# Kernel tuning notes

Hardware: AMD Instinct MI355X
Metric: run time of the kernel (lower is better)

Reference implementation:

```python
import jax, jax.numpy as jnp
import numpy as np

MAX_REL_POS = 1024


def rel_to_abs(x):
    """Music Transformer skew: [b,h,l,l] rel logits -> abs-position logits."""
    b, h, l, _ = x.shape
    x = jnp.pad(x, ((0, 0), (0, 0), (0, 0), (1, 0)))  # pad left of last dim
    x = x.reshape(b, h, l + 1, l)
    return x[:, :, 1:l + 1, :l]


def get_rel_embeddings(embed, seq_len):
    m = embed.shape[0]
    pad_len = max(seq_len - m, 0)
    start = max(m - seq_len, 0)
    padded = jnp.pad(embed, ((pad_len, 0), (0, 0)))
    return padded[start:, :]  # [seq_len, d]


def setup_inputs() -> dict:
    key = jax.random.key(0)
    kq, kk, kv, kr = jax.random.split(key, 4)
    B, H, L, D = 2, 8, 2048, 64
    # scale q so logits are O(1) (realistic attention magnitudes)
    q = jax.random.normal(kq, (B, H, L, D), dtype=jnp.float32) * (1.0 / np.sqrt(D))
    k = jax.random.normal(kk, (B, H, L, D), dtype=jnp.float32)
    v = jax.random.normal(kv, (B, H, L, D), dtype=jnp.float32)
    rel_keys_weight = jax.random.normal(kr, (MAX_REL_POS, D), dtype=jnp.float32)
    # causal mask: True = masked (masked_fill semantics)
    mask = jnp.triu(jnp.ones((L, L), dtype=bool), k=1)[None, None]
    return {"q": q, "k": k, "v": v, "rel_keys_weight": rel_keys_weight, "mask": mask}


def reference(q, k, v, rel_keys_weight, mask):
    L = q.shape[2]
    logits = jnp.einsum('bhqd,bhkd->bhqk', q, k)
    rel_keys = get_rel_embeddings(rel_keys_weight, L)          # [L, D]
    rel_logits = jnp.einsum('bhqd,md->bhqm', q, rel_keys)      # [B,H,L,L]
    logits = logits + rel_to_abs(rel_logits)
    logits = jnp.where(mask, -jnp.inf, logits)
    weights = jax.nn.softmax(logits, axis=3)
    output = jnp.matmul(weights, v)
    return (output, weights)
```

## Files before the change

kernel.cpp:

```cpp
#include <hip/hip_runtime.h>
#include <hip/hip_bf16.h>

typedef short bf16x8 __attribute__((ext_vector_type(8)));
typedef float f32x4  __attribute__((ext_vector_type(4)));

#define SEQ   2048
#define HD    64
#define LDT   72
#define TSTR  84
#define GROWS 192
#define OUT0  (16 * SEQ * HD)

__device__ __forceinline__ short f2bf(float x) {
    unsigned u = __float_as_uint(x);
    unsigned r = u + 0x7fffu + ((u >> 16) & 1u);
    return (short)(r >> 16);
}

struct F16 { float4 a[4]; };

__device__ __forceinline__ void cvt8(const float4& x, const float4& y, bf16x8& p) {
    p[0] = f2bf(x.x); p[1] = f2bf(x.y); p[2] = f2bf(x.z); p[3] = f2bf(x.w);
    p[4] = f2bf(y.x); p[5] = f2bf(y.y); p[6] = f2bf(y.z); p[7] = f2bf(y.w);
}

__device__ __forceinline__ void issue64(const float* __restrict__ base, int tid, F16& f) {
    const int r = tid >> 2, cg = tid & 3;
    const float4* src = (const float4*)(base + (size_t)r * HD + cg * 16);
#pragma unroll
    for (int t = 0; t < 4; ++t) f.a[t] = src[t];
}
__device__ __forceinline__ void write64(short* __restrict__ dst, int tid, const F16& f) {
    const int r = tid >> 2, cg = tid & 3;
    bf16x8 p0, p1;
    cvt8(f.a[0], f.a[1], p0);
    cvt8(f.a[2], f.a[3], p1);
    *(bf16x8*)&dst[r * LDT + cg * 16]     = p0;
    *(bf16x8*)&dst[r * LDT + cg * 16 + 8] = p1;
}

__device__ __forceinline__ void issueG(const float* __restrict__ eg, int tid, int etop, F16& f) {
    const int r = tid >> 2, cg = tid & 3;
    const int e = etop - r;
    if (e >= 0 && e < 1024) {
        const float4* src = (const float4*)(eg + (size_t)e * HD + cg * 16);
#pragma unroll
        for (int t = 0; t < 4; ++t) f.a[t] = src[t];
    } else {
        const float4 z = make_float4(0.f, 0.f, 0.f, 0.f);
#pragma unroll
        for (int t = 0; t < 4; ++t) f.a[t] = z;
    }
}
__device__ __forceinline__ void writeG(short* __restrict__ Gr, int tid, int sbn, const F16& f) {
    const int r = tid >> 2, cg = tid & 3;
    int sl = r + sbn; if (sl >= GROWS) sl -= GROWS;
    bf16x8 p0, p1;
    cvt8(f.a[0], f.a[1], p0);
    cvt8(f.a[2], f.a[3], p1);
    *(bf16x8*)&Gr[sl * LDT + cg * 16]     = p0;
    *(bf16x8*)&Gr[sl * LDT + cg * 16 + 8] = p1;
}

__device__ __forceinline__ void stageG_full(const float* __restrict__ eg, short* __restrict__ Gr,
                                            int tid, int i0) {
    const int dd = tid >> 1, hf = tid & 1;
    const int e = 1086 - i0 - dd;
    int sl = dd + 128; if (sl >= GROWS) sl -= GROWS;
    short* dst = &Gr[sl * LDT + hf * 32];
    if (e >= 0 && e < 1024) {
        const float4* src = (const float4*)(eg + (size_t)e * HD + hf * 32);
#pragma unroll
        for (int u = 0; u < 4; ++u) {
            bf16x8 p; cvt8(src[2 * u], src[2 * u + 1], p);
            *(bf16x8*)&dst[u * 8] = p;
        }
    } else {
        bf16x8 z = {0, 0, 0, 0, 0, 0, 0, 0};
#pragma unroll
        for (int u = 0; u < 4; ++u) *(bf16x8*)&dst[u * 8] = z;
    }
}

__device__ __forceinline__ void issueV(const float* __restrict__ vbase, int tid, F16& f) {
    const int r = tid & 63, cg = tid >> 6;
    const float4* src = (const float4*)(vbase + (size_t)r * HD + cg * 16);
#pragma unroll
    for (int t = 0; t < 4; ++t) f.a[t] = src[t];
}
__device__ __forceinline__ void writeV(short* __restrict__ Vt, int tid, const F16& f) {
    const int r = tid & 63, cg = tid >> 6;
    const float* ff = (const float*)&f.a[0];
#pragma unroll
    for (int t = 0; t < 16; ++t)
        Vt[(cg * 16 + t) * LDT + r] = f2bf(ff[t]);
}

__device__ __forceinline__ void compute_sc(const bf16x8* aq, const short* __restrict__ Ks,
                                           const short* __restrict__ Gr, int sb,
                                           int wv, int qd, int c, int lane,
                                           f32x4* sc, bool diag) {
    f32x4 tc[5];
    const f32x4 zz = {0.f, 0.f, 0.f, 0.f};
#pragma unroll
    for (int ct = 0; ct < 4; ++ct) sc[ct] = zz;
#pragma unroll
    for (int dt = 0; dt < 5; ++dt) tc[dt] = zz;
    int sl[5];
#pragma unroll
    for (int dt = 0; dt < 5; ++dt) {
        int s0 = (wv + dt) * 16 + sb + c;
        if (s0 >= GROWS) s0 -= GROWS;
        sl[dt] = s0 * LDT;
    }
#pragma unroll
    for (int s = 0; s < 2; ++s) {
        bf16x8 a = aq[s];
#pragma unroll
        for (int ct = 0; ct < 4; ++ct) {
            bf16x8 b = *(const bf16x8*)&Ks[(ct * 16 + c) * LDT + s * 32 + qd * 8];
            sc[ct] = __builtin_amdgcn_mfma_f32_16x16x32_bf16(a, b, sc[ct], 0, 0, 0);
        }
#pragma unroll
        for (int dt = 0; dt < 5; ++dt) {
            bf16x8 g = *(const bf16x8*)&Gr[sl[dt] + s * 32 + qd * 8];
            tc[dt] = __builtin_amdgcn_mfma_f32_16x16x32_bf16(a, g, tc[dt], 0, 0, 0);
        }
    }
#pragma unroll
    for (int rg = 0; rg < 4; ++rg) {
        const int rl  = qd * 4 + rg;
        const int cp  = (rl + 63 - c) & 15;
        const int src = (lane & 48) | cp;
        const bool hi = (rl + 63 - cp) >= 64;
#pragma unroll
        for (int ct = 0; ct < 4; ++ct) {
            float vs = hi ? tc[4 - ct][rg] : tc[3 - ct][rg];
            float tr = __shfl(vs, src, 64);
            float sval = sc[ct][rg] + tr;
            if (diag && (ct * 16 + c > wv * 16 + rl)) sval = -3.0e38f;
            sc[ct][rg] = sval;
        }
    }
}

__global__ __launch_bounds__(256, 2)
void relattn(const float* __restrict__ qg, const float* __restrict__ kg,
             const float* __restrict__ vg, const float* __restrict__ eg,
             float* __restrict__ outp)
{
    __shared__ short Ks2[2][64 * LDT];
    __shared__ short Gr[GROWS * LDT];
    __shared__ short Vt2[2][64 * LDT];
    __shared__ short Ps[4 * 16 * TSTR];
    __shared__ float Ls[64];

    const int tid  = threadIdx.x;
    const int wv   = tid >> 6;
    const int lane = tid & 63;
    const int qd   = lane >> 4;
    const int c    = lane & 15;

    const int bh = blockIdx.x & 15;
    const int u  = blockIdx.x >> 4;
    const int qt = (u < 16) ? u : 47 - u;
    const int i0 = qt * 64;

    float* Wg = outp + OUT0;

    {
        const int z0v = (qt + 1) * 16;
        for (int r = 0; r < 64; ++r) {
            float4* dst = (float4*)(Wg + ((size_t)(bh * SEQ + i0 + r)) * SEQ);
            for (int jv = z0v + tid; jv < SEQ / 4; jv += 256)
                dst[jv] = make_float4(0.f, 0.f, 0.f, 0.f);
        }
    }

    {
        F16 fq; issue64(qg + ((size_t)(bh * SEQ + i0)) * HD, tid, fq);
        write64(Ks2[0], tid, fq);
    }
    __syncthreads();
    bf16x8 aq[2];
#pragma unroll
    for (int s = 0; s < 2; ++s)
        aq[s] = *(const bf16x8*)&Ks2[0][(wv * 16 + c) * LDT + s * 32 + qd * 8];
    __syncthreads();

    float lrun[4];
#pragma unroll
    for (int rg = 0; rg < 4; ++rg) lrun[rg] = 0.f;

    f32x4 ob[4];
    {
        const f32x4 zz = {0.f, 0.f, 0.f, 0.f};
#pragma unroll
        for (int dt = 0; dt < 4; ++dt) ob[dt] = zz;
    }

    {
        F16 fk; issue64(kg + ((size_t)(bh * SEQ)) * HD, tid, fk);
        write64(Ks2[0], tid, fk);
        stageG_full(eg, Gr, tid, i0);
        F16 fv; issueV(vg + ((size_t)(bh * SEQ)) * HD, tid, fv);
        writeV(Vt2[0], tid, fv);
    }
    __syncthreads();
    int sb = 128;
    short* Pw = &Ps[wv * 16 * TSTR];
    for (int kt = 0; kt <= qt; ++kt) {
        const int cur = kt & 1;
        const bool pf = kt < qt;
        const int sbn = (sb >= 64) ? sb - 64 : sb + 128;
        const int j0 = kt * 64;
        F16 fk, fg, fv;
        if (pf) {
            issue64(kg + ((size_t)(bh * SEQ + j0 + 64)) * HD, tid, fk);
            issueG(eg, tid, 1086 - i0 + j0 + 64, fg);
            issueV(vg + ((size_t)(bh * SEQ + j0 + 64)) * HD, tid, fv);
        }
        f32x4 sc[4];
        compute_sc(aq, Ks2[cur], Gr, sb, wv, qd, c, lane, sc, kt == qt);

#pragma unroll
        for (int rg = 0; rg < 4; ++rg) {
            const int rl = qd * 4 + rg;
            const int ig = i0 + wv * 16 + rl;
            float* wrow = Wg + ((size_t)(bh * SEQ + ig)) * SEQ + j0;
            float p[4];
#pragma unroll
            for (int ct = 0; ct < 4; ++ct) {
                p[ct] = __expf(sc[ct][rg]);
                wrow[ct * 16 + c] = p[ct];
                Pw[rl * TSTR + ct * 16 + c] = f2bf(p[ct]);
            }
            float ss = (p[0] + p[1]) + (p[2] + p[3]);
            ss += __shfl_xor(ss, 1);
            ss += __shfl_xor(ss, 2);
            ss += __shfl_xor(ss, 4);
            ss += __shfl_xor(ss, 8);
            lrun[rg] += ss;
        }

#pragma unroll
        for (int s = 0; s < 2; ++s) {
            bf16x8 ap = *(const bf16x8*)&Pw[c * TSTR + s * 32 + qd * 8];
#pragma unroll
            for (int dt = 0; dt < 4; ++dt) {
                bf16x8 bv = *(const bf16x8*)&Vt2[cur][(dt * 16 + c) * LDT + s * 32 + qd * 8];
                ob[dt] = __builtin_amdgcn_mfma_f32_16x16x32_bf16(ap, bv, ob[dt], 0, 0, 0);
            }
        }
        if (pf) {
            write64(Ks2[cur ^ 1], tid, fk);
            writeG(Gr, tid, sbn, fg);
            writeV(Vt2[cur ^ 1], tid, fv);
        }
        sb = sbn;
        __syncthreads();
    }

    float linv[4];
#pragma unroll
    for (int rg = 0; rg < 4; ++rg) linv[rg] = 1.0f / lrun[rg];

    if (c == 0) {
#pragma unroll
        for (int rg = 0; rg < 4; ++rg)
            Ls[wv * 16 + qd * 4 + rg] = linv[rg];
    }
    __syncthreads();

    {
        const int w16 = (qt + 1) * 16;
        for (int r = 0; r < 64; ++r) {
            const float s = Ls[r];
            float4* dst = (float4*)(Wg + ((size_t)(bh * SEQ + i0 + r)) * SEQ);
            for (int jv = tid; jv < w16; jv += 256) {
                float4 w = dst[jv];
                w.x *= s; w.y *= s; w.z *= s; w.w *= s;
                dst[jv] = w;
            }
        }
    }

#pragma unroll
    for (int dt = 0; dt < 4; ++dt)
#pragma unroll
        for (int rg = 0; rg < 4; ++rg) {
            const int ig = i0 + wv * 16 + qd * 4 + rg;
            outp[((size_t)(bh * SEQ + ig)) * HD + dt * 16 + c] = ob[dt][rg] * linv[rg];
        }
}

extern "C" void kernel_launch(void* const* d_in, const int* in_sizes, int n_in,
                              void* d_out, int out_size, void* d_ws, size_t ws_size,
                              hipStream_t stream) {
    const float* q = (const float*)d_in[0];
    const float* k = (const float*)d_in[1];
    const float* v = (const float*)d_in[2];
    const float* e = (const float*)d_in[3];
    float* out = (float*)d_out;
    hipLaunchKernelGGL(relattn, dim3(512), dim3(256), 0, stream, q, k, v, e, out);
}
```

Measured before the change: 448.5 us.

## Use two-pass softmax to write normalized weights directly, with key-split 512-thread blocks

The kernel now runs a first pass that only accumulates the exp row sums. A second pass recomputes the logits and writes already-normalized weights, which removes the read-modify-write rescale sweep over the large weights output. Each block now has 8 waves that split every 128-key block into two 64-key halves, and their partial sums and outputs are combined through LDS. Each block handles a complementary pair of query tiles to balance the causal workload. The cost is computing the QK and relative-logit MFMAs twice, plus one 512-thread block per CU with new LDS strides and setprio hints.

```diff
diff --git a/kernel.cpp b/kernel.cpp
--- a/kernel.cpp
+++ b/kernel.cpp
@@ -6,9 +6,10 @@
 
 #define SEQ   2048
 #define HD    64
-#define LDT   72
-#define TSTR  84
-#define GROWS 192
+#define LDT   66
+#define VSTR  130
+#define PSTR  66
+#define GROWS 320
 #define OUT0  (16 * SEQ * HD)
 
 __device__ __forceinline__ short f2bf(float x) {
@@ -17,20 +18,26 @@
     return (short)(r >> 16);
 }
 
-struct F16 { float4 a[4]; };
-
 __device__ __forceinline__ void cvt8(const float4& x, const float4& y, bf16x8& p) {
     p[0] = f2bf(x.x); p[1] = f2bf(x.y); p[2] = f2bf(x.z); p[3] = f2bf(x.w);
     p[4] = f2bf(y.x); p[5] = f2bf(y.y); p[6] = f2bf(y.z); p[7] = f2bf(y.w);
 }
 
-__device__ __forceinline__ void issue64(const float* __restrict__ base, int tid, F16& f) {
+__device__ __forceinline__ void barrier_lds() {
+    asm volatile("s_waitcnt lgkmcnt(0)" ::: "memory");
+    __builtin_amdgcn_s_barrier();
+    asm volatile("" ::: "memory");
+}
+
+struct F16 { float4 a[4]; };
+
+__device__ __forceinline__ void issueK(const float* __restrict__ base, int tid, F16& f) {
     const int r = tid >> 2, cg = tid & 3;
     const float4* src = (const float4*)(base + (size_t)r * HD + cg * 16);
 #pragma unroll
     for (int t = 0; t < 4; ++t) f.a[t] = src[t];
 }
-__device__ __forceinline__ void write64(short* __restrict__ dst, int tid, const F16& f) {
+__device__ __forceinline__ void writeK(short* __restrict__ dst, int tid, const F16& f) {
     const int r = tid >> 2, cg = tid & 3;
     bf16x8 p0, p1;
     cvt8(f.a[0], f.a[1], p0);
@@ -39,9 +46,9 @@
     *(bf16x8*)&dst[r * LDT + cg * 16 + 8] = p1;
 }
 
-__device__ __forceinline__ void issueG(const float* __restrict__ eg, int tid, int etop, F16& f) {
+__device__ __forceinline__ void issueG(const float* __restrict__ eg, int tid, int emax, F16& f) {
     const int r = tid >> 2, cg = tid & 3;
-    const int e = etop - r;
+    const int e = emax - r;
     if (e >= 0 && e < 1024) {
         const float4* src = (const float4*)(eg + (size_t)e * HD + cg * 16);
 #pragma unroll
@@ -63,62 +70,63 @@
 }
 
 __device__ __forceinline__ void stageG_full(const float* __restrict__ eg, short* __restrict__ Gr,
-                                            int tid, int i0) {
-    const int dd = tid >> 1, hf = tid & 1;
-    const int e = 1086 - i0 - dd;
-    int sl = dd + 128; if (sl >= GROWS) sl -= GROWS;
-    short* dst = &Gr[sl * LDT + hf * 32];
-    if (e >= 0 && e < 1024) {
-        const float4* src = (const float4*)(eg + (size_t)e * HD + hf * 32);
-#pragma unroll
-        for (int u = 0; u < 4; ++u) {
-            bf16x8 p; cvt8(src[2 * u], src[2 * u + 1], p);
-            *(bf16x8*)&dst[u * 8] = p;
-        }
-    } else {
-        bf16x8 z = {0, 0, 0, 0, 0, 0, 0, 0};
-#pragma unroll
-        for (int u = 0; u < 4; ++u) *(bf16x8*)&dst[u * 8] = z;
+                                            int tid, int emax0) {
+    const int r0 = tid >> 3, cg8 = tid & 7;
+#pragma unroll
+    for (int u = 0; u < 3; ++u) {
+        const int x = u * 64 + r0;
+        const int e = emax0 - x;
+        short* dst = &Gr[(x + 128) * LDT + cg8 * 8];
+        if (e >= 0 && e < 1024) {
+            const float4* src = (const float4*)(eg + (size_t)e * HD + cg8 * 8);
+            bf16x8 p; cvt8(src[0], src[1], p);
+            *(bf16x8*)dst = p;
+        } else {
+            bf16x8 z = {0, 0, 0, 0, 0, 0, 0, 0};
+            *(bf16x8*)dst = z;
+        }
     }
 }
 
 __device__ __forceinline__ void issueV(const float* __restrict__ vbase, int tid, F16& f) {
-    const int r = tid & 63, cg = tid >> 6;
-    const float4* src = (const float4*)(vbase + (size_t)r * HD + cg * 16);
+    const int r3 = tid & 127, dg = (tid >> 7) * 16;
+    const float4* src = (const float4*)(vbase + (size_t)r3 * HD + dg);
 #pragma unroll
     for (int t = 0; t < 4; ++t) f.a[t] = src[t];
 }
 __device__ __forceinline__ void writeV(short* __restrict__ Vt, int tid, const F16& f) {
-    const int r = tid & 63, cg = tid >> 6;
+    const int r3 = tid & 127, dg = (tid >> 7) * 16;
     const float* ff = (const float*)&f.a[0];
 #pragma unroll
     for (int t = 0; t < 16; ++t)
-        Vt[(cg * 16 + t) * LDT + r] = f2bf(ff[t]);
+        Vt[(dg + t) * VSTR + r3] = f2bf(ff[t]);
 }
 
 __device__ __forceinline__ void compute_sc(const bf16x8* aq, const short* __restrict__ Ks,
                                            const short* __restrict__ Gr, int sb,
-                                           int wv, int qd, int c, int lane,
-                                           f32x4* sc, bool diag) {
+                                           int w4, int jhh, int qd, int c, int lane,
+                                           f32x4* sc , bool diag, int igq, int jgq) {
     f32x4 tc[5];
     const f32x4 zz = {0.f, 0.f, 0.f, 0.f};
 #pragma unroll
     for (int ct = 0; ct < 4; ++ct) sc[ct] = zz;
 #pragma unroll
     for (int dt = 0; dt < 5; ++dt) tc[dt] = zz;
+    const int X0 = w4 * 16 - jhh + 64;
     int sl[5];
 #pragma unroll
     for (int dt = 0; dt < 5; ++dt) {
-        int s0 = (wv + dt) * 16 + sb + c;
+        int s0 = X0 + dt * 16 + c + sb;
         if (s0 >= GROWS) s0 -= GROWS;
         sl[dt] = s0 * LDT;
     }
+    __builtin_amdgcn_s_setprio(1);
 #pragma unroll
     for (int s = 0; s < 2; ++s) {
         bf16x8 a = aq[s];
 #pragma unroll
         for (int ct = 0; ct < 4; ++ct) {
-            bf16x8 b = *(const bf16x8*)&Ks[(ct * 16 + c) * LDT + s * 32 + qd * 8];
+            bf16x8 b = *(const bf16x8*)&Ks[(jhh + ct * 16 + c) * LDT + s * 32 + qd * 8];
             sc[ct] = __builtin_amdgcn_mfma_f32_16x16x32_bf16(a, b, sc[ct], 0, 0, 0);
         }
 #pragma unroll
@@ -127,171 +135,217 @@
             tc[dt] = __builtin_amdgcn_mfma_f32_16x16x32_bf16(a, g, tc[dt], 0, 0, 0);
         }
     }
+    __builtin_amdgcn_s_setprio(0);
 #pragma unroll
     for (int rg = 0; rg < 4; ++rg) {
         const int rl  = qd * 4 + rg;
-        const int cp  = (rl + 63 - c) & 15;
+        const int cp  = (rl + 15 - c) & 15;
         const int src = (lane & 48) | cp;
-        const bool hi = (rl + 63 - cp) >= 64;
+        const bool hi = rl > cp;
 #pragma unroll
         for (int ct = 0; ct < 4; ++ct) {
             float vs = hi ? tc[4 - ct][rg] : tc[3 - ct][rg];
             float tr = __shfl(vs, src, 64);
             float sval = sc[ct][rg] + tr;
-            if (diag && (ct * 16 + c > wv * 16 + rl)) sval = -3.0e38f;
+            if (diag && (jgq + ct * 16 + c > igq + rl)) sval = -3.0e38f;
             sc[ct][rg] = sval;
         }
     }
 }
 
-__global__ __launch_bounds__(256, 2)
+__global__ __launch_bounds__(512, 2)
 void relattn(const float* __restrict__ qg, const float* __restrict__ kg,
              const float* __restrict__ vg, const float* __restrict__ eg,
              float* __restrict__ outp)
 {
-    __shared__ short Ks2[2][64 * LDT];
+    __shared__ short Ks2[2][128 * LDT];
     __shared__ short Gr[GROWS * LDT];
-    __shared__ short Vt2[2][64 * LDT];
-    __shared__ short Ps[4 * 16 * TSTR];
-    __shared__ float Ls[64];
+    __shared__ short Vt2[2][64 * VSTR];
+    __shared__ short Ps[8 * 16 * PSTR];
+    __shared__ float Lp[2][64];
 
     const int tid  = threadIdx.x;
     const int wv   = tid >> 6;
     const int lane = tid & 63;
     const int qd   = lane >> 4;
     const int c    = lane & 15;
+    const int w4   = wv & 3;
+    const int jhh  = (wv >> 2) * 64;
 
     const int bh = blockIdx.x & 15;
-    const int u  = blockIdx.x >> 4;
-    const int qt = (u < 16) ? u : 47 - u;
-    const int i0 = qt * 64;
+    const int pp = blockIdx.x >> 4;
 
     float* Wg = outp + OUT0;
 
-    {
-        const int z0v = (qt + 1) * 16;
-        for (int r = 0; r < 64; ++r) {
-            float4* dst = (float4*)(Wg + ((size_t)(bh * SEQ + i0 + r)) * SEQ);
-            for (int jv = z0v + tid; jv < SEQ / 4; jv += 256)
-                dst[jv] = make_float4(0.f, 0.f, 0.f, 0.f);
-        }
-    }
-
-    {
-        F16 fq; issue64(qg + ((size_t)(bh * SEQ + i0)) * HD, tid, fq);
-        write64(Ks2[0], tid, fq);
-    }
-    __syncthreads();
-    bf16x8 aq[2];
-#pragma unroll
-    for (int s = 0; s < 2; ++s)
-        aq[s] = *(const bf16x8*)&Ks2[0][(wv * 16 + c) * LDT + s * 32 + qd * 8];
-    __syncthreads();
-
-    float lrun[4];
-#pragma unroll
-    for (int rg = 0; rg < 4; ++rg) lrun[rg] = 0.f;
-
-    f32x4 ob[4];
-    {
-        const f32x4 zz = {0.f, 0.f, 0.f, 0.f};
-#pragma unroll
-        for (int dt = 0; dt < 4; ++dt) ob[dt] = zz;
-    }
-
-    {
-        F16 fk; issue64(kg + ((size_t)(bh * SEQ)) * HD, tid, fk);
-        write64(Ks2[0], tid, fk);
-        stageG_full(eg, Gr, tid, i0);
-        F16 fv; issueV(vg + ((size_t)(bh * SEQ)) * HD, tid, fv);
-        writeV(Vt2[0], tid, fv);
-    }
-    __syncthreads();
-    int sb = 128;
-    short* Pw = &Ps[wv * 16 * TSTR];
-    for (int kt = 0; kt <= qt; ++kt) {
-        const int cur = kt & 1;
-        const bool pf = kt < qt;
-        const int sbn = (sb >= 64) ? sb - 64 : sb + 128;
-        const int j0 = kt * 64;
-        F16 fk, fg, fv;
-        if (pf) {
-            issue64(kg + ((size_t)(bh * SEQ + j0 + 64)) * HD, tid, fk);
-            issueG(eg, tid, 1086 - i0 + j0 + 64, fg);
-            issueV(vg + ((size_t)(bh * SEQ + j0 + 64)) * HD, tid, fv);
-        }
-        f32x4 sc[4];
-        compute_sc(aq, Ks2[cur], Gr, sb, wv, qd, c, lane, sc, kt == qt);
+    for (int half = 0; half < 2; ++half) {
+        const int qt = half ? pp : (31 - pp);
+        const int i0 = qt * 64;
+        const int nb = (qt + 2) >> 1;
+
+        __syncthreads();
+
+        {
+            const int z0v = nb * 32;
+            for (int r = 0; r < 64; ++r) {
+                float4* dst = (float4*)(Wg + ((size_t)(bh * SEQ + i0 + r)) * SEQ);
+                for (int jv = z0v + tid; jv < SEQ / 4; jv += 512)
+                    dst[jv] = make_float4(0.f, 0.f, 0.f, 0.f);
+            }
+        }
+
+        {
+            const int r = tid >> 3, cg8 = tid & 7;
+            const float4* src = (const float4*)(qg + ((size_t)(bh * SEQ + i0 + r)) * HD + cg8 * 8);
+            bf16x8 p; cvt8(src[0], src[1], p);
+            *(bf16x8*)&Ks2[0][r * LDT + cg8 * 8] = p;
+        }
+        __syncthreads();
+        bf16x8 aq[2];
+#pragma unroll
+        for (int s = 0; s < 2; ++s)
+            aq[s] = *(const bf16x8*)&Ks2[0][(w4 * 16 + c) * LDT + s * 32 + qd * 8];
+        __syncthreads();
+
+        float lrun[4];
+#pragma unroll
+        for (int rg = 0; rg < 4; ++rg) lrun[rg] = 0.f;
+
+        {
+            F16 fk; issueK(kg + ((size_t)(bh * SEQ)) * HD, tid, fk);
+            writeK(Ks2[0], tid, fk);
+            stageG_full(eg, Gr, tid, 1150 - i0);
+        }
+        __syncthreads();
+        int sb = 128;
+        for (int kb = 0; kb < nb; ++kb) {
+            const int cur = kb & 1;
+            const bool pf = kb + 1 < nb;
+            const int sbn = (sb >= 128) ? sb - 128 : sb + 192;
+            F16 fk, fg;
+            if (pf) {
+                issueK(kg + ((size_t)(bh * SEQ + (kb + 1) * 128)) * HD, tid, fk);
+                issueG(eg, tid, 1150 - i0 + (kb + 1) * 128, fg);
+            }
+            f32x4 sc[4];
+            compute_sc(aq, Ks2[cur], Gr, sb, w4, jhh, qd, c, lane, sc,
+                       kb == nb - 1, i0 + w4 * 16, kb * 128 + jhh);
+#pragma unroll
+            for (int rg = 0; rg < 4; ++rg)
+                lrun[rg] += (__expf(sc[0][rg]) + __expf(sc[1][rg]))
+                          + (__expf(sc[2][rg]) + __expf(sc[3][rg]));
+            if (pf) {
+                writeK(Ks2[cur ^ 1], tid, fk);
+                writeG(Gr, tid, sbn, fg);
+            }
+            sb = sbn;
+            barrier_lds();
+        }
 
 #pragma unroll
         for (int rg = 0; rg < 4; ++rg) {
-            const int rl = qd * 4 + rg;
-            const int ig = i0 + wv * 16 + rl;
-            float* wrow = Wg + ((size_t)(bh * SEQ + ig)) * SEQ + j0;
-            float p[4];
-#pragma unroll
-            for (int ct = 0; ct < 4; ++ct) {
-                p[ct] = __expf(sc[ct][rg]);
-                wrow[ct * 16 + c] = p[ct];
-                Pw[rl * TSTR + ct * 16 + c] = f2bf(p[ct]);
-            }
-            float ss = (p[0] + p[1]) + (p[2] + p[3]);
+            float ss = lrun[rg];
             ss += __shfl_xor(ss, 1);
             ss += __shfl_xor(ss, 2);
             ss += __shfl_xor(ss, 4);
             ss += __shfl_xor(ss, 8);
-            lrun[rg] += ss;
-        }
-
-#pragma unroll
-        for (int s = 0; s < 2; ++s) {
-            bf16x8 ap = *(const bf16x8*)&Pw[c * TSTR + s * 32 + qd * 8];
-#pragma unroll
-            for (int dt = 0; dt < 4; ++dt) {
-                bf16x8 bv = *(const bf16x8*)&Vt2[cur][(dt * 16 + c) * LDT + s * 32 + qd * 8];
-                ob[dt] = __builtin_amdgcn_mfma_f32_16x16x32_bf16(ap, bv, ob[dt], 0, 0, 0);
-            }
-        }
-        if (pf) {
-            write64(Ks2[cur ^ 1], tid, fk);
-            writeG(Gr, tid, sbn, fg);
-            writeV(Vt2[cur ^ 1], tid, fv);
-        }
-        sb = sbn;
-        __syncthreads();
-    }
-
-    float linv[4];
-#pragma unroll
-    for (int rg = 0; rg < 4; ++rg) linv[rg] = 1.0f / lrun[rg];
-
-    if (c == 0) {
-#pragma unroll
-        for (int rg = 0; rg < 4; ++rg)
-            Ls[wv * 16 + qd * 4 + rg] = linv[rg];
-    }
-    __syncthreads();
-
-    {
-        const int w16 = (qt + 1) * 16;
-        for (int r = 0; r < 64; ++r) {
-            const float s = Ls[r];
-            float4* dst = (float4*)(Wg + ((size_t)(bh * SEQ + i0 + r)) * SEQ);
-            for (int jv = tid; jv < w16; jv += 256) {
-                float4 w = dst[jv];
-                w.x *= s; w.y *= s; w.z *= s; w.w *= s;
-                dst[jv] = w;
-            }
-        }
-    }
-
-#pragma unroll
-    for (int dt = 0; dt < 4; ++dt)
+            lrun[rg] = ss;
+        }
+        if (c == 0) {
+#pragma unroll
+            for (int rg = 0; rg < 4; ++rg)
+                Lp[wv >> 2][w4 * 16 + qd * 4 + rg] = lrun[rg];
+        }
+        __syncthreads();
+        float linv[4];
 #pragma unroll
         for (int rg = 0; rg < 4; ++rg) {
-            const int ig = i0 + wv * 16 + qd * 4 + rg;
-            outp[((size_t)(bh * SEQ + ig)) * HD + dt * 16 + c] = ob[dt][rg] * linv[rg];
-        }
+            const int row = w4 * 16 + qd * 4 + rg;
+            linv[rg] = 1.0f / (Lp[0][row] + Lp[1][row]);
+        }
+
+        f32x4 ob[4];
+        {
+            const f32x4 zz = {0.f, 0.f, 0.f, 0.f};
+#pragma unroll
+            for (int dt = 0; dt < 4; ++dt) ob[dt] = zz;
+        }
+
+        {
+            F16 fk; issueK(kg + ((size_t)(bh * SEQ)) * HD, tid, fk);
+            writeK(Ks2[0], tid, fk);
+            stageG_full(eg, Gr, tid, 1150 - i0);
+            F16 fv; issueV(vg + ((size_t)(bh * SEQ)) * HD, tid, fv);
+            writeV(Vt2[0], tid, fv);
+        }
+        __syncthreads();
+        sb = 128;
+        short* Pw = &Ps[wv * 16 * PSTR];
+        for (int kb = 0; kb < nb; ++kb) {
+            const int cur = kb & 1;
+            const bool pf = kb + 1 < nb;
+            const int sbn = (sb >= 128) ? sb - 128 : sb + 192;
+            const int j0 = kb * 128;
+            F16 fk, fg, fv;
+            if (pf) {
+                issueK(kg + ((size_t)(bh * SEQ + j0 + 128)) * HD, tid, fk);
+                issueG(eg, tid, 1150 - i0 + j0 + 128, fg);
+                issueV(vg + ((size_t)(bh * SEQ + j0 + 128)) * HD, tid, fv);
+            }
+            f32x4 sc[4];
+            compute_sc(aq, Ks2[cur], Gr, sb, w4, jhh, qd, c, lane, sc,
+                       kb == nb - 1, i0 + w4 * 16, j0 + jhh);
+
+#pragma unroll
+            for (int rg = 0; rg < 4; ++rg) {
+                const int rl = qd * 4 + rg;
+                const int ig = i0 + w4 * 16 + rl;
+                float* wrow = Wg + ((size_t)(bh * SEQ + ig)) * SEQ + j0 + jhh;
+#pragma unroll
+                for (int ct = 0; ct < 4; ++ct) {
+                    const float w = __expf(sc[ct][rg]) * linv[rg];
+                    wrow[ct * 16 + c] = w;
+                    Pw[rl * PSTR + ct * 16 + c] = f2bf(w);
+                }
+            }
+
+#pragma unroll
+            for (int s = 0; s < 2; ++s) {
+                bf16x8 ap = *(const bf16x8*)&Pw[c * PSTR + s * 32 + qd * 8];
+#pragma unroll
+                for (int dt = 0; dt < 4; ++dt) {
+                    bf16x8 bv = *(const bf16x8*)&Vt2[cur][(dt * 16 + c) * VSTR + jhh + s * 32 + qd * 8];
+                    ob[dt] = __builtin_amdgcn_mfma_f32_16x16x32_bf16(ap, bv, ob[dt], 0, 0, 0);
+                }
+            }
+            if (pf) {
+                writeK(Ks2[cur ^ 1], tid, fk);
+                writeG(Gr, tid, sbn, fg);
+                writeV(Vt2[cur ^ 1], tid, fv);
+            }
+            sb = sbn;
+            barrier_lds();
+        }
+
+        float* Oc = (float*)&Ks2[0][0];
+        if (jhh == 0) {
+#pragma unroll
+            for (int dt = 0; dt < 4; ++dt)
+#pragma unroll
+                for (int rg = 0; rg < 4; ++rg)
+                    Oc[(w4 * 16 + qd * 4 + rg) * 66 + dt * 16 + c] = ob[dt][rg];
+        }
+        __syncthreads();
+        if (jhh == 64) {
+#pragma unroll
+            for (int dt = 0; dt < 4; ++dt)
+#pragma unroll
+                for (int rg = 0; rg < 4; ++rg) {
+                    const int ig = i0 + w4 * 16 + qd * 4 + rg;
+                    const float val = ob[dt][rg] + Oc[(w4 * 16 + qd * 4 + rg) * 66 + dt * 16 + c];
+                    outp[((size_t)(bh * SEQ + ig)) * HD + dt * 16 + c] = val;
+                }
+        }
+    }
 }
 
 extern "C" void kernel_launch(void* const* d_in, const int* in_sizes, int n_in,
@@ -302,5 +356,5 @@
     const float* v = (const float*)d_in[2];
     const float* e = (const float*)d_in[3];
     float* out = (float*)d_out;
-    hipLaunchKernelGGL(relattn, dim3(512), dim3(256), 0, stream, q, k, v, e, out);
-}
+    hipLaunchKernelGGL(relattn, dim3(256), dim3(512), 0, stream, q, k, v, e, out);
+}
```

Measured after the change: 487.5 us. 1.09x slower.
